# Optimization experiments

Measured on AMD Instinct MI355X. Metric: run time of the kernel, lower is better.

## Reference

```python
import jax, jax.numpy as jnp
import numpy as np

TOPK = 8
N_EXPERTS = 64
ROUTE_SCALE = 1.0


def setup_inputs() -> dict:
    key = jax.random.key(0)
    k1, k2 = jax.random.split(key)
    x = jax.random.normal(k1, (16, 256, 64, 64), dtype=jnp.float32)
    gate_w = jax.random.normal(k2, (64, 256, 3, 3), dtype=jnp.float32) * 0.02  # [E, C, kh, kw]
    bias = jnp.zeros((64,), dtype=jnp.float32)  # load-balancing bias buffer
    return {"x": x, "gate_w": gate_w, "bias": bias}


def reference(x, gate_w, bias):
    # 3x3 conv, stride 1, pad 1 (SAME), no conv bias -> expert logits [B, E, H, W]
    logits = jax.lax.conv_general_dilated(
        x, gate_w, window_strides=(1, 1), padding="SAME",
        dimension_numbers=("NCHW", "OIHW", "NCHW"))
    scores = jax.nn.sigmoid(logits)                 # [B, E, H, W]
    s = jnp.moveaxis(scores, 1, -1)                 # [B, H, W, E]
    biased = s + bias                               # bias broadcast over experts
    _, idx = jax.lax.top_k(biased, TOPK)            # [B, H, W, K] (topk on biased scores)
    w = jnp.take_along_axis(s, idx, axis=-1)        # gather UNbiased scores
    w = jax.nn.softmax(w, axis=-1) * ROUTE_SCALE    # softmax over the K selected experts
    weights = jnp.moveaxis(w, -1, 1)                # [B, K, H, W] to match torch layout
    indices = jnp.moveaxis(idx, -1, 1)              # [B, K, H, W]
    counts = jnp.zeros((N_EXPERTS,), jnp.int32).at[idx.ravel()].add(1)  # bincount
    return weights, indices, counts
```

## Files before the change

kernel.cpp:

```cpp
#include <hip/hip_runtime.h>


typedef _Float16 half8 __attribute__((ext_vector_type(8)));
typedef __attribute__((ext_vector_type(4))) float f32x4;

#define LOG2E 1.44269504f

__device__ __forceinline__ unsigned short f2h_bits(float f) {
    _Float16 h = (_Float16)f;
    unsigned short b;
    __builtin_memcpy(&b, &h, 2);
    return b;
}

constexpr int WB_U4 = 8 * 9 * 4 * 64;
constexpr size_t XT_BYTES = (size_t)16 * 66 * 8 * 66 * 32 * 2;
constexpr size_t WS_NEED  = XT_BYTES + (size_t)WB_U4 * 16 + 262144;


constexpr int NB_INT = 4096, NB_BOR = 130, NB_WB = 72;
constexpr int PREP_GRID = NB_INT + NB_BOR + NB_WB;

__global__ __launch_bounds__(256) void prep_all2(
    const float* __restrict__ x, const float* __restrict__ gw,
    _Float16* __restrict__ xT, unsigned short* __restrict__ wB,
    float* __restrict__ out) {
    const int blk = blockIdx.x, tid = threadIdx.x;
    if (blk < NB_INT) {
        int gid = blk * 256 + tid;
        int w = gid & 63, c16 = (gid >> 6) & 15, h = (gid >> 10) & 63, b = gid >> 16;
        int c0 = c16 * 16;
        const float* src = x + ((b * 256 + c0) * 64 + h) * 64 + w;
        float v[16];
#pragma unroll
        for (int j = 0; j < 16; ++j) v[j] = src[j * 4096];
        uint4 p0, p1;
        p0.x = (unsigned)f2h_bits(v[0])  | ((unsigned)f2h_bits(v[1])  << 16);
        p0.y = (unsigned)f2h_bits(v[2])  | ((unsigned)f2h_bits(v[3])  << 16);
        p0.z = (unsigned)f2h_bits(v[4])  | ((unsigned)f2h_bits(v[5])  << 16);
        p0.w = (unsigned)f2h_bits(v[6])  | ((unsigned)f2h_bits(v[7])  << 16);
        p1.x = (unsigned)f2h_bits(v[8])  | ((unsigned)f2h_bits(v[9])  << 16);
        p1.y = (unsigned)f2h_bits(v[10]) | ((unsigned)f2h_bits(v[11]) << 16);
        p1.z = (unsigned)f2h_bits(v[12]) | ((unsigned)f2h_bits(v[13]) << 16);
        p1.w = (unsigned)f2h_bits(v[14]) | ((unsigned)f2h_bits(v[15]) << 16);
        int q = c16 >> 1;
        size_t idx = ((((size_t)b * 66 + h + 1) * 8 + q) * 66 + (w + 1)) * 32
                     + (c16 & 1) * 16;
        uint4* dst = (uint4*)(xT + idx);
        dst[0] = p0; dst[1] = p1;
    } else if (blk < NB_INT + NB_BOR) {
        int t = (blk - NB_INT) * 256 + tid;
        int q = t & 7, site = t >> 3;
        int sb = site / 260, s = site - sb * 260;
        int hp, wp;
        if (s < 132) { hp = (s >= 66) ? 65 : 0; wp = (s >= 66) ? (s - 66) : s; }
        else         { int s2 = s - 132; hp = 1 + (s2 >> 1); wp = (s2 & 1) * 65; }
        uint4 z = {0u, 0u, 0u, 0u};
        size_t idx = ((((size_t)sb * 66 + hp) * 8 + q) * 66 + wp) * 32;
        uint4* dst = (uint4*)(xT + idx);
#pragma unroll
        for (int k = 0; k < 4; ++k) dst[k] = z;
    } else {
        int wblk = blk - (NB_INT + NB_BOR);
        if (wblk == 0 && tid < 64) out[1048576 + tid] = 0.f;
        int g = wblk * 256 + tid;
        int lane = g & 63;
        int nt   = (g >> 6) & 3;
        int rest = g >> 8;
        int t = rest % 9, q = rest / 9;
        int e  = nt * 16 + (lane & 15);
        int c0 = q * 32 + (lane >> 4) * 8;
        unsigned short o[8];
#pragma unroll
        for (int j = 0; j < 8; ++j)
            o[j] = f2h_bits(gw[(e * 256 + c0 + j) * 9 + t]);
        uint4 pk;
        pk.x = (unsigned)o[0] | ((unsigned)o[1] << 16);
        pk.y = (unsigned)o[2] | ((unsigned)o[3] << 16);
        pk.z = (unsigned)o[4] | ((unsigned)o[5] << 16);
        pk.w = (unsigned)o[6] | ((unsigned)o[7] << 16);
        ((uint4*)wB)[g] = pk;
    }
}

constexpr int SSTR = 68;
constexpr int QSTR = 66 * 32;

__global__ __launch_bounds__(256, 4) void gate_main3(
    const _Float16* __restrict__ xT, const float* __restrict__ bias,
    const unsigned short* __restrict__ wB, float* __restrict__ out) {
    __shared__ float scf[64 * SSTR];
    __shared__ float bias_s[64];
    __shared__ int   hist[64];

    const int tid  = threadIdx.x;
    const int lane = tid & 63;
    const int rw   = tid >> 6;
    const int blk  = blockIdx.x;
    const int b    = blk & 15;
    const int r    = blk >> 4;

    if (tid < 64) { bias_s[tid] = bias[tid]; hist[tid] = 0; }

    const int ph = rw >> 1, eh = rw & 1;

    const _Float16* pa[3];
#pragma unroll
    for (int kh = 0; kh < 3; ++kh)
        pa[kh] = xT + ((((size_t)b * 66 + r + kh) * 8) * 66
                       + ph * 32 + (lane & 15)) * 32 + (lane >> 4) * 8;

    const uint4* bptr = (const uint4*)wB + eh * 128 + lane;

    half8 Aa[3][2];
    uint4 Bb[6][2];
    f32x4 acc[2][2];
#pragma unroll
    for (int mt = 0; mt < 2; ++mt)
#pragma unroll
        for (int nt = 0; nt < 2; ++nt) acc[mt][nt] = (f32x4){0.f, 0.f, 0.f, 0.f};

    auto lda = [&](int t, int slot) {
        const int kh = t / 3, kw = t % 3;
#pragma unroll
        for (int m = 0; m < 2; ++m)
            Aa[slot][m] = *(const half8*)(pa[kh] + (m * 16 + kw) * 32);
    };
    auto ldb = [&](int slot) {
#pragma unroll
        for (int nt = 0; nt < 2; ++nt) Bb[slot][nt] = bptr[nt * 64];
        bptr += 256;
    };
    auto mt_ = [&](int as, int bs) {
#pragma unroll
        for (int nt = 0; nt < 2; ++nt) {
            half8 bfr;
            __builtin_memcpy(&bfr, &Bb[bs][nt], 16);
#pragma unroll
            for (int m = 0; m < 2; ++m)
                acc[m][nt] = __builtin_amdgcn_mfma_f32_16x16x32_f16(
                    Aa[as][m], bfr, acc[m][nt], 0, 0, 0);
        }
    };
    auto bump = [&]() {
#pragma unroll
        for (int kh = 0; kh < 3; ++kh) pa[kh] += QSTR;
    };
    auto SB = []() { __builtin_amdgcn_sched_barrier(0); };

    lda(0, 0); lda(1, 1); lda(2, 2);
    ldb(0); ldb(1); ldb(2); ldb(3); ldb(4); ldb(5);
    SB();

#pragma unroll 1
    for (int i = 0; i < 4; ++i) {
        mt_(0, 0); lda(3, 0); ldb(0); SB();
        mt_(1, 1); lda(4, 1); ldb(1); SB();
        mt_(2, 2); lda(5, 2); ldb(2); SB();
        mt_(0, 3); lda(6, 0); ldb(3); SB();
        mt_(1, 4); lda(7, 1); ldb(4); SB();
        mt_(2, 5); lda(8, 2); ldb(5); SB();
        bump();
        mt_(0, 0); lda(0, 0); ldb(0); SB();
        mt_(1, 1); lda(1, 1); ldb(1); SB();
        mt_(2, 2); lda(2, 2); ldb(2); SB();
        mt_(0, 3); lda(3, 0); ldb(3); SB();
        mt_(1, 4); lda(4, 1); ldb(4); SB();
        mt_(2, 5); lda(5, 2); ldb(5); SB();
        mt_(0, 0); lda(6, 0); ldb(0); SB();
        mt_(1, 1); lda(7, 1); ldb(1); SB();
        mt_(2, 2); lda(8, 2); ldb(2); SB();
        bump();
        mt_(0, 3); lda(0, 0); ldb(3); SB();
        mt_(1, 4); lda(1, 1); ldb(4); SB();
        mt_(2, 5); lda(2, 2); ldb(5); SB();
    }

#pragma unroll
    for (int mt = 0; mt < 2; ++mt)
#pragma unroll
        for (int nt = 0; nt < 2; ++nt)
#pragma unroll
            for (int rr = 0; rr < 4; ++rr) {
                float v = acc[mt][nt][rr];
                float s = 1.f / (1.f + __builtin_amdgcn_exp2f(-v * LOG2E));
                int p = ph * 32 + mt * 16 + ((lane >> 4) << 2) + rr;
                int e = eh * 32 + nt * 16 + (lane & 15);
                scf[p * SSTR + e] = s;
            }
    __syncthreads();

    if (tid < 64) {
        const float* row = scf + tid * SSTR;
        float tv[8];
        int   ti[8];
#pragma unroll
        for (int k = 0; k < 8; ++k) { tv[k] = -3.0e38f; ti[k] = 0; }
#pragma unroll
        for (int j4 = 0; j4 < 16; ++j4) {
            f32x4 blkv = *(const f32x4*)(row + j4 * 4);
#pragma unroll
            for (int j = 0; j < 4; ++j) {
                int   e  = j4 * 4 + j;
                float bs = blkv[j] + bias_s[e];
                if (bs > tv[7]) {
                    tv[7] = bs; ti[7] = e;
#pragma unroll
                    for (int k = 7; k > 0; --k) {
                        float fa = tv[k - 1], fb = tv[k];
                        int   ia = ti[k - 1], ib = ti[k];
                        bool  sw = fb > fa;
                        tv[k - 1] = sw ? fb : fa; tv[k] = sw ? fa : fb;
                        ti[k - 1] = sw ? ib : ia; ti[k] = sw ? ia : ib;
                    }
                }
            }
        }
        float u[8], mx = -3.0e38f;
#pragma unroll
        for (int k = 0; k < 8; ++k) { u[k] = tv[k] - bias_s[ti[k]]; mx = fmaxf(mx, u[k]); }
        float ex[8], sum = 0.f;
#pragma unroll
        for (int k = 0; k < 8; ++k) { ex[k] = __builtin_amdgcn_exp2f((u[k] - mx) * LOG2E); sum += ex[k]; }
        float inv = 1.f / sum;

        int obase = b * 32768 + r * 64 + tid;
#pragma unroll
        for (int k = 0; k < 8; ++k) {
            out[obase + k * 4096]          = ex[k] * inv;
            out[524288 + obase + k * 4096] = (float)ti[k];
            atomicAdd(&hist[ti[k]], 1);
        }
    }
    __syncthreads();
    if (tid < 64) atomicAdd(out + 1048576 + tid, (float)hist[tid]);
}


__global__ __launch_bounds__(256) void gate_prep(const float* __restrict__ gw,
                                                 unsigned short* __restrict__ wB,
                                                 float* __restrict__ out) {
    int g = blockIdx.x * 256 + threadIdx.x;
    if (blockIdx.x == 0 && threadIdx.x < 64) out[1048576 + threadIdx.x] = 0.f;
    if (g >= WB_U4) return;
    int lane = g & 63;
    int nt   = (g >> 6) & 3;
    int rest = g >> 8;
    int t = rest % 9, q = rest / 9;
    int e  = nt * 16 + (lane & 15);
    int c0 = q * 32 + (lane >> 4) * 8;
    unsigned short o[8];
#pragma unroll
    for (int j = 0; j < 8; ++j)
        o[j] = f2h_bits(gw[(e * 256 + c0 + j) * 9 + t]);
    uint4 pk;
    pk.x = (unsigned)o[0] | ((unsigned)o[1] << 16);
    pk.y = (unsigned)o[2] | ((unsigned)o[3] << 16);
    pk.z = (unsigned)o[4] | ((unsigned)o[5] << 16);
    pk.w = (unsigned)o[6] | ((unsigned)o[7] << 16);
    ((uint4*)wB)[g] = pk;
}

constexpr int CSTR = 40;
constexpr int SLAB = 3 * 66 * CSTR;

__global__ __launch_bounds__(256, 4) void gate_main_fb(
    const float* __restrict__ x, const float* __restrict__ bias,
    const unsigned short* __restrict__ wB, float* __restrict__ out) {
    __shared__ unsigned short xs[2 * SLAB];
    __shared__ float bias_s[64];
    __shared__ int   hist[64];

    const int tid  = threadIdx.x;
    const int lane = tid & 63;
    const int rw   = tid >> 6;
    const int blk  = blockIdx.x;
    const int b    = blk & 15;
    const int r    = blk >> 4;

    if (tid < 64) { bias_s[tid] = bias[tid]; hist[tid] = 0; }
    {
        uint4 z = {0u, 0u, 0u, 0u};
        uint4* p = (uint4*)xs;
#pragma unroll
        for (int i = 0; i < 8; ++i) {
            int idx = tid + i * 256;
            if (idx < 2 * SLAB / 8) p[idx] = z;
        }
    }

    bool tOk[4];
    int  tSrc[4], tDst[4];
#pragma unroll
    for (int i = 0; i < 4; ++i) {
        int T = tid + i * 256;
        bool ex = (T < 792);
        int chh = T / 198, s = T - chh * 198;
        int row2 = s / 66, wp = s - row2 * 66;
        int gr = r - 1 + row2, gwc = wp - 1;
        tOk[i]  = ex && (gr >= 0) && (gr < 64) && (gwc >= 0) && (gwc < 64);
        tSrc[i] = ((b * 256 + chh * 8) * 64 + gr) * 64 + gwc;
        tDst[i] = (row2 * 66 + wp) * CSTR + chh * 8;
    }

    float tb[4][8];
    auto issueT = [&](int i, int dq) {
        if (tOk[i]) {
            const float* p = x + tSrc[i] + dq * 131072;
#pragma unroll
            for (int u = 0; u < 8; ++u) tb[i][u] = p[u * 4096];
        }
    };
    auto commitT = [&](int i, unsigned short* dst) {
        if (tOk[i]) {
            uint4 pk;
            pk.x = (unsigned)f2h_bits(tb[i][0]) | ((unsigned)f2h_bits(tb[i][1]) << 16);
            pk.y = (unsigned)f2h_bits(tb[i][2]) | ((unsigned)f2h_bits(tb[i][3]) << 16);
            pk.z = (unsigned)f2h_bits(tb[i][4]) | ((unsigned)f2h_bits(tb[i][5]) << 16);
            pk.w = (unsigned)f2h_bits(tb[i][6]) | ((unsigned)f2h_bits(tb[i][7]) << 16);
            *(uint4*)(dst + tDst[i]) = pk;
        }
    };

    const int ph = rw >> 1, eh = rw & 1;
    half8 Aa[3][2];
    uint4 Bb[3][2];
    auto prefA = [&](const unsigned short* buf, int t, int slot) {
        const int kh = t / 3, kw = t % 3;
        const unsigned short* abase =
            buf + (kh * 66 + ph * 32 + (lane & 15) + kw) * CSTR + (lane >> 4) * 8;
#pragma unroll
        for (int mt = 0; mt < 2; ++mt)
            Aa[slot][mt] = *(const half8*)(abase + mt * 16 * CSTR);
    };
    auto prefB = [&](int T9, int slot) {
        const uint4* bp = (const uint4*)wB + (T9 * 4 + eh * 2) * 64 + lane;
#pragma unroll
        for (int nt = 0; nt < 2; ++nt) Bb[slot][nt] = bp[nt * 64];
    };

    f32x4 acc[2][2];
#pragma unroll
    for (int mt = 0; mt < 2; ++mt)
#pragma unroll
        for (int nt = 0; nt < 2; ++nt) acc[mt][nt] = (f32x4){0.f, 0.f, 0.f, 0.f};

    auto mfma_tap = [&](int slot) {
#pragma unroll
        for (int nt = 0; nt < 2; ++nt) {
            half8 bfr;
            __builtin_memcpy(&bfr, &Bb[slot][nt], 16);
#pragma unroll
            for (int mt = 0; mt < 2; ++mt)
                acc[mt][nt] = __builtin_amdgcn_mfma_f32_16x16x32_f16(
                    Aa[slot][mt], bfr, acc[mt][nt], 0, 0, 0);
        }
    };

    __syncthreads();
    issueT(0, 0); issueT(1, 0); issueT(2, 0); issueT(3, 0);
    commitT(0, xs); commitT(1, xs); commitT(2, xs); commitT(3, xs);
    issueT(0, 1); issueT(1, 1); issueT(2, 1); issueT(3, 1);
    prefB(0, 0); prefB(1, 1); prefB(2, 2);
    __syncthreads();

#pragma unroll 1
    for (int q = 0; q < 8; ++q) {
        const unsigned short* cur = xs + (q & 1) * SLAB;
        unsigned short*       nxt = xs + ((q + 1) & 1) * SLAB;
        const int  T0  = q * 9;
        const bool cmt = (q < 7);
        const bool iss = (q < 6);

        prefA(cur, 0, 0); prefA(cur, 1, 1);
        mfma_tap(0); prefB(T0 + 3, 0); prefA(cur, 2, 2);
        mfma_tap(1); prefB(T0 + 4, 1); prefA(cur, 3, 0);
        if (cmt) { commitT(0, nxt); commitT(1, nxt); }
        mfma_tap(2); prefB(T0 + 5, 2); prefA(cur, 4, 1);
        mfma_tap(0); prefB(T0 + 6, 0); prefA(cur, 5, 2);
        if (cmt) { commitT(2, nxt); commitT(3, nxt); }
        mfma_tap(1); prefB(T0 + 7, 1); prefA(cur, 6, 0);
        mfma_tap(2); prefB(T0 + 8, 2); prefA(cur, 7, 1);
        __builtin_amdgcn_sched_barrier(0);
        if (iss) { issueT(0, q + 2); issueT(1, q + 2); issueT(2, q + 2); issueT(3, q + 2); }
        __builtin_amdgcn_sched_barrier(0);
        mfma_tap(0); if (cmt) prefB(T0 + 9, 0);  prefA(cur, 8, 2);
        mfma_tap(1); if (cmt) prefB(T0 + 10, 1);
        mfma_tap(2); if (cmt) prefB(T0 + 11, 2);
        __syncthreads();
    }

    float* scf2 = (float*)xs;
#pragma unroll
    for (int mt = 0; mt < 2; ++mt)
#pragma unroll
        for (int nt = 0; nt < 2; ++nt)
#pragma unroll
            for (int rr = 0; rr < 4; ++rr) {
                float v = acc[mt][nt][rr];
                float s = 1.f / (1.f + __builtin_amdgcn_exp2f(-v * LOG2E));
                int p = ph * 32 + mt * 16 + ((lane >> 4) << 2) + rr;
                int e = eh * 32 + nt * 16 + (lane & 15);
                scf2[p * SSTR + e] = s;
            }
    __syncthreads();

    if (tid < 64) {
        const float* row = scf2 + tid * SSTR;
        float tv[8];
        int   ti[8];
#pragma unroll
        for (int k = 0; k < 8; ++k) { tv[k] = -3.0e38f; ti[k] = 0; }
#pragma unroll
        for (int j4 = 0; j4 < 16; ++j4) {
            f32x4 blkv = *(const f32x4*)(row + j4 * 4);
#pragma unroll
            for (int j = 0; j < 4; ++j) {
                int   e  = j4 * 4 + j;
                float bs = blkv[j] + bias_s[e];
                if (bs > tv[7]) {
                    tv[7] = bs; ti[7] = e;
#pragma unroll
                    for (int k = 7; k > 0; --k) {
                        float fa = tv[k - 1], fb = tv[k];
                        int   ia = ti[k - 1], ib = ti[k];
                        bool  sw = fb > fa;
                        tv[k - 1] = sw ? fb : fa; tv[k] = sw ? fa : fb;
                        ti[k - 1] = sw ? ib : ia; ti[k] = sw ? ia : ib;
                    }
                }
            }
        }
        float u[8], mx = -3.0e38f;
#pragma unroll
        for (int k = 0; k < 8; ++k) { u[k] = tv[k] - bias_s[ti[k]]; mx = fmaxf(mx, u[k]); }
        float ex[8], sum = 0.f;
#pragma unroll
        for (int k = 0; k < 8; ++k) { ex[k] = __builtin_amdgcn_exp2f((u[k] - mx) * LOG2E); sum += ex[k]; }
        float inv = 1.f / sum;

        int obase = b * 32768 + r * 64 + tid;
#pragma unroll
        for (int k = 0; k < 8; ++k) {
            out[obase + k * 4096]          = ex[k] * inv;
            out[524288 + obase + k * 4096] = (float)ti[k];
            atomicAdd(&hist[ti[k]], 1);
        }
    }
    __syncthreads();
    if (tid < 64) atomicAdd(out + 1048576 + tid, (float)hist[tid]);
}

extern "C" void kernel_launch(void* const* d_in, const int* in_sizes, int n_in,
                              void* d_out, int out_size, void* d_ws, size_t ws_size,
                              hipStream_t stream) {
    const float* x    = (const float*)d_in[0];
    const float* gw   = (const float*)d_in[1];
    const float* bias = (const float*)d_in[2];
    float* out = (float*)d_out;

    if (ws_size >= WS_NEED) {
        _Float16* xT = (_Float16*)d_ws;
        unsigned short* wB = (unsigned short*)((char*)d_ws + XT_BYTES);
        prep_all2<<<PREP_GRID, 256, 0, stream>>>(x, gw, xT, wB, out);
        gate_main3<<<1024, 256, 0, stream>>>(xT, bias, wB, out);
    } else {
        unsigned short* wB = (unsigned short*)d_ws;
        gate_prep<<<72, 256, 0, stream>>>(gw, wB, out);
        gate_main_fb<<<1024, 256, 0, stream>>>(x, bias, wB, out);
    }
}
```

Measured before the change: 172.6 us.

## Stage input rows through LDS with double-buffered async global-to-LDS loads

The main gate kernel now copies the three padded input rows for each channel chunk into shared memory with asynchronous global_load_lds, double-buffered across two halves, instead of every wave reading its A fragments straight from global memory. Each A fragment is then read from LDS at the right kh/kw offset, so the overlapping 3x3 window reads are served from on-chip memory rather than repeated global loads. Prefetch of the next chunk overlaps the MFMA work, and hand-placed waitcnt counters plus barriers order the two buffers. This raises shared memory use and adds barriers, which may cost occupancy, and it depends on the manual vmcnt values being correct.

```diff
diff --git a/kernel.cpp b/kernel.cpp
--- a/kernel.cpp
+++ b/kernel.cpp
@@ -16,6 +16,11 @@
 constexpr int WB_U4 = 8 * 9 * 4 * 64;
 constexpr size_t XT_BYTES = (size_t)16 * 66 * 8 * 66 * 32 * 2;
 constexpr size_t WS_NEED  = XT_BYTES + (size_t)WB_U4 * 16 + 262144;
+
+#define GLOAD16(gp, lp)                                                    \
+    __builtin_amdgcn_global_load_lds(                                      \
+        (const __attribute__((address_space(1))) void*)(gp),               \
+        (__attribute__((address_space(3))) void*)(lp), 16, 0, 0)
 
 
 constexpr int NB_INT = 4096, NB_BOR = 130, NB_WB = 72;
@@ -84,14 +89,15 @@
 }
 
 constexpr int SSTR = 68;
-constexpr int QSTR = 66 * 32;
-
-__global__ __launch_bounds__(256, 4) void gate_main3(
+constexpr int HALFB = 12672;
+
+__global__ __launch_bounds__(256, 4) void gate_main4(
     const _Float16* __restrict__ xT, const float* __restrict__ bias,
     const unsigned short* __restrict__ wB, float* __restrict__ out) {
-    __shared__ float scf[64 * SSTR];
+    __shared__ uint4 smem4[2 * HALFB / 16];
     __shared__ float bias_s[64];
     __shared__ int   hist[64];
+    char* smem = (char*)smem4;
 
     const int tid  = threadIdx.x;
     const int lane = tid & 63;
@@ -104,14 +110,26 @@
 
     const int ph = rw >> 1, eh = rw & 1;
 
-    const _Float16* pa[3];
-#pragma unroll
-    for (int kh = 0; kh < 3; ++kh)
-        pa[kh] = xT + ((((size_t)b * 66 + r + kh) * 8) * 66
-                       + ph * 32 + (lane & 15)) * 32 + (lane >> 4) * 8;
-
-    const uint4* bptr = (const uint4*)wB + eh * 128 + lane;
-
+    const _Float16* srcP[4];
+    int ldsOff[4];
+    const bool act3 = (tid < 24);
+#pragma unroll
+    for (int i = 0; i < 4; ++i) {
+        int T = tid + i * 256;
+        if (T >= 792) T = 0;
+        int seg = T / 264, o = T - seg * 264;
+        srcP[i]  = xT + ((size_t)(b * 66 + r + seg) * 8) * 2112 + o * 8;
+        ldsOff[i] = T * 16;
+    }
+    auto STAGE = [&](int q, int halfB) {
+#pragma unroll
+        for (int i = 0; i < 3; ++i)
+            GLOAD16(srcP[i] + q * 2112, smem + ldsOff[i] + halfB);
+        if (act3)
+            GLOAD16(srcP[3] + q * 2112, smem + ldsOff[3] + halfB);
+    };
+
+    const char* aP0 = smem + ((ph * 32 + (lane & 15)) * 64 + (lane >> 4) * 16);
     half8 Aa[3][2];
     uint4 Bb[6][2];
     f32x4 acc[2][2];
@@ -120,18 +138,17 @@
 #pragma unroll
         for (int nt = 0; nt < 2; ++nt) acc[mt][nt] = (f32x4){0.f, 0.f, 0.f, 0.f};
 
-    auto lda = [&](int t, int slot) {
-        const int kh = t / 3, kw = t % 3;
-#pragma unroll
-        for (int m = 0; m < 2; ++m)
-            Aa[slot][m] = *(const half8*)(pa[kh] + (m * 16 + kw) * 32);
-    };
-    auto ldb = [&](int slot) {
-#pragma unroll
-        for (int nt = 0; nt < 2; ++nt) Bb[slot][nt] = bptr[nt * 64];
-        bptr += 256;
-    };
-    auto mt_ = [&](int as, int bs) {
+    auto LDA = [&](int kh, int kw, int slot, int HB) {
+        Aa[slot][0] = *(const half8*)(aP0 + HB + kh * 4224 + kw * 64);
+        Aa[slot][1] = *(const half8*)(aP0 + HB + kh * 4224 + kw * 64 + 1024);
+    };
+    const char* bP = (const char*)wB + eh * 2048 + lane * 16;
+    auto LDB = [&](int slot) {
+        Bb[slot][0] = *(const uint4*)bP;
+        Bb[slot][1] = *(const uint4*)(bP + 1024);
+        bP += 4096;
+    };
+    auto MT = [&](int as, int bs) {
 #pragma unroll
         for (int nt = 0; nt < 2; ++nt) {
             half8 bfr;
@@ -142,40 +159,55 @@
                     Aa[as][m], bfr, acc[m][nt], 0, 0, 0);
         }
     };
-    auto bump = [&]() {
-#pragma unroll
-        for (int kh = 0; kh < 3; ++kh) pa[kh] += QSTR;
-    };
     auto SB = []() { __builtin_amdgcn_sched_barrier(0); };
 
-    lda(0, 0); lda(1, 1); lda(2, 2);
-    ldb(0); ldb(1); ldb(2); ldb(3); ldb(4); ldb(5);
+    STAGE(0, 0);
+    LDB(0); LDB(1); LDB(2); LDB(3); LDB(4); LDB(5);
+    SB();
+    asm volatile("s_waitcnt vmcnt(12)" ::: "memory");
+    __builtin_amdgcn_s_barrier();
     SB();
 
 #pragma unroll 1
     for (int i = 0; i < 4; ++i) {
-        mt_(0, 0); lda(3, 0); ldb(0); SB();
-        mt_(1, 1); lda(4, 1); ldb(1); SB();
-        mt_(2, 2); lda(5, 2); ldb(2); SB();
-        mt_(0, 3); lda(6, 0); ldb(3); SB();
-        mt_(1, 4); lda(7, 1); ldb(4); SB();
-        mt_(2, 5); lda(8, 2); ldb(5); SB();
-        bump();
-        mt_(0, 0); lda(0, 0); ldb(0); SB();
-        mt_(1, 1); lda(1, 1); ldb(1); SB();
-        mt_(2, 2); lda(2, 2); ldb(2); SB();
-        mt_(0, 3); lda(3, 0); ldb(3); SB();
-        mt_(1, 4); lda(4, 1); ldb(4); SB();
-        mt_(2, 5); lda(5, 2); ldb(5); SB();
-        mt_(0, 0); lda(6, 0); ldb(0); SB();
-        mt_(1, 1); lda(7, 1); ldb(1); SB();
-        mt_(2, 2); lda(8, 2); ldb(2); SB();
-        bump();
-        mt_(0, 3); lda(0, 0); ldb(3); SB();
-        mt_(1, 4); lda(1, 1); ldb(4); SB();
-        mt_(2, 5); lda(2, 2); ldb(5); SB();
-    }
-
+        STAGE(2 * i + 1, HALFB);
+        LDA(0, 0, 0, 0); LDA(0, 1, 1, 0); LDA(0, 2, 2, 0);
+        SB();
+        MT(0, 0); LDA(1, 0, 0, 0); LDB(0); SB();
+        MT(1, 1); LDA(1, 1, 1, 0); LDB(1); SB();
+        MT(2, 2); LDA(1, 2, 2, 0); LDB(2); SB();
+        MT(0, 3); LDA(2, 0, 0, 0); LDB(3); SB();
+        MT(1, 4); LDA(2, 1, 1, 0); LDB(4); SB();
+        MT(2, 5); LDA(2, 2, 2, 0); LDB(5); SB();
+        MT(0, 0); LDB(0); SB();
+        MT(1, 1); LDB(1); SB();
+        MT(2, 2); LDB(2); SB();
+        SB();
+        asm volatile("s_waitcnt vmcnt(18) lgkmcnt(0)" ::: "memory");
+        __builtin_amdgcn_s_barrier();
+        SB();
+        if (i < 3) STAGE(2 * i + 2, 0);
+        LDA(0, 0, 0, HALFB); LDA(0, 1, 1, HALFB); LDA(0, 2, 2, HALFB);
+        SB();
+        MT(0, 3); LDA(1, 0, 0, HALFB); LDB(3); SB();
+        MT(1, 4); LDA(1, 1, 1, HALFB); LDB(4); SB();
+        MT(2, 5); LDA(1, 2, 2, HALFB); LDB(5); SB();
+        MT(0, 0); LDA(2, 0, 0, HALFB); LDB(0); SB();
+        MT(1, 1); LDA(2, 1, 1, HALFB); LDB(1); SB();
+        MT(2, 2); LDA(2, 2, 2, HALFB); LDB(2); SB();
+        MT(0, 3); LDB(3); SB();
+        MT(1, 4); LDB(4); SB();
+        MT(2, 5); LDB(5); SB();
+        if (i < 3) {
+            SB();
+            asm volatile("s_waitcnt vmcnt(18) lgkmcnt(0)" ::: "memory");
+            __builtin_amdgcn_s_barrier();
+            SB();
+        }
+    }
+    __syncthreads();
+
+    float* scf = (float*)smem4;
 #pragma unroll
     for (int mt = 0; mt < 2; ++mt)
 #pragma unroll
@@ -463,7 +495,7 @@
         _Float16* xT = (_Float16*)d_ws;
         unsigned short* wB = (unsigned short*)((char*)d_ws + XT_BYTES);
         prep_all2<<<PREP_GRID, 256, 0, stream>>>(x, gw, xT, wB, out);
-        gate_main3<<<1024, 256, 0, stream>>>(xT, bias, wB, out);
+        gate_main4<<<1024, 256, 0, stream>>>(xT, bias, wB, out);
     } else {
         unsigned short* wB = (unsigned short*)d_ws;
         gate_prep<<<72, 256, 0, stream>>>(gw, wB, out);
```

Result: faster. 155.0 us (-10.2%).
